# Performance work log

Measured on AMD Instinct MI355X. Metric: run time of the kernel, lower is better.

## Reference

```python
import jax, jax.numpy as jnp
import numpy as np

COST_KEYPOINT = 1.0
COST_GIOU = 1.0


def box_cxcyczwhd_to_xyzxyz(b):
    c, s = b[..., :3], b[..., 3:]
    return jnp.concatenate([c - 0.5 * s, c + 0.5 * s], axis=-1)


def generalized_3d_box_iou(b1, b2):
    # b1: [N,6], b2: [M,6], both xyzxyz. Returns [N,M] GIoU.
    vol1 = jnp.prod(b1[:, 3:] - b1[:, :3], axis=-1)
    vol2 = jnp.prod(b2[:, 3:] - b2[:, :3], axis=-1)
    lt = jnp.maximum(b1[:, None, :3], b2[None, :, :3])
    rb = jnp.minimum(b1[:, None, 3:], b2[None, :, 3:])
    inter = jnp.prod(jnp.maximum(rb - lt, 0.0), axis=-1)
    union = vol1[:, None] + vol2[None, :] - inter
    iou = inter / union
    elt = jnp.minimum(b1[:, None, :3], b2[None, :, :3])
    erb = jnp.maximum(b1[:, None, 3:], b2[None, :, 3:])
    evol = jnp.prod(jnp.maximum(erb - elt, 0.0), axis=-1)
    return iou - (evol - union) / evol


@jax.jit
def compute_cost(pred_keypoints, pred_boxes, tgt_boxes, tgt_keypoints):
    bs, Q = pred_keypoints.shape[:2]
    out_kp = pred_keypoints.reshape(bs * Q, -1)            # [bs*Q, K*3]
    out_boxes = pred_boxes.reshape(bs * Q, 6)
    tgt_b = tgt_boxes.reshape(-1, 6)                        # [T_total, 6]
    tgt_kp = tgt_keypoints.reshape(tgt_b.shape[0], -1)      # [T_total, K*3]
    xyz_min = box_cxcyczwhd_to_xyzxyz(tgt_b)[:, :3]
    K3 = tgt_kp.shape[-1]
    kp = tgt_kp.reshape(-1, K3 // 3, 3)
    # normalize keypoints relative to box min-corner and box size
    dist_kp = ((kp - xyz_min[:, None, :]) / tgt_b[:, None, 3:]).reshape(-1, K3)
    # L1 cdist: [bs*Q, T_total]
    cost_kp = jnp.sum(jnp.abs(out_kp[:, None, :] - dist_kp[None, :, :]), axis=-1)
    cost_giou = -generalized_3d_box_iou(
        box_cxcyczwhd_to_xyzxyz(out_boxes), box_cxcyczwhd_to_xyzxyz(tgt_b))
    C = COST_KEYPOINT * cost_kp + COST_GIOU * cost_giou
    return C.reshape(bs, Q, -1)


def _lap(cost):
    # Jonker-Volgenant shortest-augmenting-path LAP (scipy-style).
    # cost: [n, m] with n <= m. Returns (arange(n), col4row).
    cost = np.asarray(cost, dtype=np.float64)
    n, m = cost.shape
    u = np.zeros(n)
    v = np.zeros(m)
    col4row = np.full(n, -1, np.int64)
    row4col = np.full(m, -1, np.int64)
    for curRow in range(n):
        path = np.full(m, -1, np.int64)
        SR = np.zeros(n, bool)
        SC = np.zeros(m, bool)
        shortest = np.full(m, np.inf)
        minVal = 0.0
        i = curRow
        sink = -1
        while sink == -1:
            SR[i] = True
            idx = np.where(~SC)[0]
            r = minVal + cost[i, idx] - u[i] - v[idx]
            better = r < shortest[idx]
            shortest[idx[better]] = r[better]
            path[idx[better]] = i
            jloc = np.argmin(shortest[idx])
            j = idx[jloc]
            minVal = shortest[j]
            SC[j] = True
            if row4col[j] == -1:
                sink = j
            else:
                i = row4col[j]
        u[curRow] += minVal
        mask = SR.copy()
        mask[curRow] = False
        u[mask] += minVal - shortest[col4row[mask]]
        v[SC] -= minVal - shortest[SC]
        j = sink
        while True:
            i = path[j]
            row4col[j] = i
            col4row[i], j = j, col4row[i]
            if i == curRow:
                break
    return np.arange(n), col4row


def _linear_sum_assignment(cost):
    # cost: [Q, T] with Q >= T; mirrors scipy's transpose handling:
    # returns (row_ind sorted ascending, matching col_ind).
    rows, cols = _lap(cost.T)  # rows = arange(T) targets, cols = query ids
    order = np.argsort(cols)
    return cols[order], rows[order]


def setup_inputs() -> dict:
    key = jax.random.key(0)
    k1, k2, k3, k4, k5, k6 = jax.random.split(key, 6)
    BS, Q, T, K = 16, 300, 50, 17
    pred_keypoints = jax.random.normal(k1, (BS, Q, K * 3), dtype=jnp.float32)
    pred_boxes = jnp.concatenate([
        jax.random.uniform(k2, (BS, Q, 3), dtype=jnp.float32),
        jax.random.uniform(k3, (BS, Q, 3), dtype=jnp.float32) * 0.5 + 0.05,
    ], axis=-1)
    tgt_boxes = jnp.concatenate([
        jax.random.uniform(k4, (BS, T, 3), dtype=jnp.float32),
        jax.random.uniform(k5, (BS, T, 3), dtype=jnp.float32) * 0.5 + 0.05,
    ], axis=-1)
    tgt_keypoints = jax.random.uniform(k6, (BS, T, K * 3), dtype=jnp.float32)
    return {"pred_keypoints": pred_keypoints, "pred_boxes": pred_boxes,
            "tgt_boxes": tgt_boxes, "tgt_keypoints": tgt_keypoints}


def reference(pred_keypoints, pred_boxes, tgt_boxes, tgt_keypoints):
    C = compute_cost(pred_keypoints, pred_boxes, tgt_boxes, tgt_keypoints)
    Cn = np.asarray(C)
    bs, Q, _ = Cn.shape
    T = tgt_boxes.shape[1]
    # per-image block of the column-split cost matrix, as in torch C.split(sizes, -1)
    idx = []
    for b in range(bs):
        i, j = _linear_sum_assignment(Cn[b, :, b * T:(b + 1) * T])
        idx.append(np.stack([i, j]))
    indices = jnp.asarray(np.stack(idx), dtype=jnp.int32)  # [bs, 2, T]
    return C, indices
```

## Files before the change

kernel.cpp:

```cpp
#include <hip/hip_runtime.h>
#include <math.h>

#define BSZ 16
#define NQ 300
#define NT 50
#define K3 51
#define NPRED (BSZ*NQ)
#define NTGT  (BSZ*NT)
#define NC    (NPRED*NTGT)

template<int CTRL, int RMASK>
__device__ __forceinline__ double dpp_minstep_f64(double x) {
    long long bb = __double_as_longlong(x);
    int lo = (int)(bb & 0xFFFFFFFFll);
    int hi = (int)(bb >> 32);
    int mlo = __builtin_amdgcn_update_dpp(lo, lo, CTRL, RMASK, 0xF, false);
    int mhi = __builtin_amdgcn_update_dpp(hi, hi, CTRL, RMASK, 0xF, false);
    double other = __longlong_as_double(((long long)mhi << 32) | (long long)(unsigned)mlo);
    return fmin(x, other);
}
__device__ __forceinline__ double wave_min_f64(double x) {
    x = dpp_minstep_f64<0xB1, 0xF>(x);
    x = dpp_minstep_f64<0x4E, 0xF>(x);
    x = dpp_minstep_f64<0x141, 0xF>(x);
    x = dpp_minstep_f64<0x140, 0xF>(x);
    x = dpp_minstep_f64<0x142, 0xA>(x);
    x = dpp_minstep_f64<0x143, 0xC>(x);
    long long bb = __double_as_longlong(x);
    int lo = __builtin_amdgcn_readlane((int)(bb & 0xFFFFFFFFll), 63);
    int hi = __builtin_amdgcn_readlane((int)(bb >> 32), 63);
    return __longlong_as_double(((long long)hi << 32) | (long long)(unsigned)lo);
}
template<int CTRL, int RMASK>
__device__ __forceinline__ float dpp_minstep_f32(float x) {
    int m = __builtin_amdgcn_update_dpp(__float_as_int(x), __float_as_int(x), CTRL, RMASK, 0xF, false);
    return fminf(x, __int_as_float(m));
}
__device__ __forceinline__ float wave_min_f32(float x) {
    x = dpp_minstep_f32<0xB1, 0xF>(x);
    x = dpp_minstep_f32<0x4E, 0xF>(x);
    x = dpp_minstep_f32<0x141, 0xF>(x);
    x = dpp_minstep_f32<0x140, 0xF>(x);
    x = dpp_minstep_f32<0x142, 0xA>(x);
    x = dpp_minstep_f32<0x143, 0xC>(x);
    return __int_as_float(__builtin_amdgcn_readlane(__float_as_int(x), 63));
}
__device__ __forceinline__ double readlane_f64(double x, int lane) {
    long long bb = __double_as_longlong(x);
    int lo = __builtin_amdgcn_readlane((int)(bb & 0xFFFFFFFFll), lane);
    int hi = __builtin_amdgcn_readlane((int)(bb >> 32), lane);
    return __longlong_as_double(((long long)hi << 32) | (long long)(unsigned)lo);
}

__device__ __forceinline__ float giou_cost(
    float plt0, float plt1, float plt2, float prb0, float prb1, float prb2, float pvol,
    float tlt0, float tlt1, float tlt2, float trb0, float trb1, float trb2, float tvol)
{
    float inter = fmaxf(fminf(prb0,trb0) - fmaxf(plt0,tlt0), 0.f);
    inter *= fmaxf(fminf(prb1,trb1) - fmaxf(plt1,tlt1), 0.f);
    inter *= fmaxf(fminf(prb2,trb2) - fmaxf(plt2,tlt2), 0.f);
    float evol = fmaxf(fmaxf(prb0,trb0) - fminf(plt0,tlt0), 0.f);
    evol *= fmaxf(fmaxf(prb1,trb1) - fminf(plt1,tlt1), 0.f);
    evol *= fmaxf(fmaxf(prb2,trb2) - fminf(plt2,tlt2), 0.f);
    float uni = pvol + tvol - inter;
    return inter/uni - (evol - uni)/evol;
}

__global__ __launch_bounds__(1024) void cost_kernel(
    const float* __restrict__ pred_kp, const float* __restrict__ pred_boxes,
    const float* __restrict__ tgt_boxes, const float* __restrict__ tgt_kp,
    float* __restrict__ C, float* __restrict__ wsT)
{
    __shared__ __align__(16) float s_dk[80*56];
    __shared__ float s_tbox[80*12];
    __shared__ float s_pk[64*K3];

    const int cb = blockIdx.x;
    const int pb = cb % 75, tb = cb / 75;
    const int p0 = pb * 64, t0 = tb * 80;
    const int tid = threadIdx.x;

    if (tid < 80) {
        const float* tb6 = tgt_boxes + (size_t)(t0 + tid) * 6;
        float c0=tb6[0], c1=tb6[1], c2=tb6[2], s0=tb6[3], s1=tb6[4], s2=tb6[5];
        float l0=c0-0.5f*s0, l1=c1-0.5f*s1, l2=c2-0.5f*s2;
        float r0=c0+0.5f*s0, r1=c1+0.5f*s1, r2=c2+0.5f*s2;
        float* tw = s_tbox + tid*12;
        tw[0]=l0; tw[1]=l1; tw[2]=l2; tw[3]=r0; tw[4]=r1; tw[5]=r2;
        tw[6]=(r0-l0)*(r1-l1)*(r2-l2);
        tw[9]=s0; tw[10]=s1; tw[11]=s2;
    }
    __syncthreads();
    for (int e = tid; e < 80*K3; e += 1024) {
        int t = e / K3; int c = e - t*K3; int d = c % 3;
        float kp = tgt_kp[(size_t)t0*K3 + e];
        s_dk[t*56 + c] = (kp - s_tbox[t*12 + d]) / s_tbox[t*12 + 9 + d];
    }
    for (int e = tid; e < 64*K3; e += 1024)
        s_pk[e] = pred_kp[(size_t)p0*K3 + e];
    __syncthreads();

    const int pl = tid & 63, g = tid >> 6;
    float a[K3];
    #pragma unroll
    for (int c = 0; c < K3; ++c) a[c] = s_pk[pl*K3 + c];
    const int p = p0 + pl;
    const float* pb6 = pred_boxes + (size_t)p * 6;
    float pc0=pb6[0],pc1=pb6[1],pc2=pb6[2],ps0=pb6[3],ps1=pb6[4],ps2=pb6[5];
    float plt0=pc0-0.5f*ps0, plt1=pc1-0.5f*ps1, plt2=pc2-0.5f*ps2;
    float prb0=pc0+0.5f*ps0, prb1=pc1+0.5f*ps1, prb2=pc2+0.5f*ps2;
    float pvol=(prb0-plt0)*(prb1-plt1)*(prb2-plt2);
    const int bb2  = p / NQ;
    const int prel = p - bb2*NQ;

    #pragma unroll
    for (int k = 0; k < 5; ++k) {
        int tl = g*5 + k;
        const float* bbp = s_dk + tl*56;
        float sum = 0.f;
        #pragma unroll
        for (int c4 = 0; c4 < 12; ++c4) {
            float4 q = *(const float4*)(bbp + 4*c4);
            sum += fabsf(a[4*c4+0] - q.x);
            sum += fabsf(a[4*c4+1] - q.y);
            sum += fabsf(a[4*c4+2] - q.z);
            sum += fabsf(a[4*c4+3] - q.w);
        }
        sum += fabsf(a[48] - bbp[48]);
        sum += fabsf(a[49] - bbp[49]);
        sum += fabsf(a[50] - bbp[50]);
        const float* tw = s_tbox + tl*12;
        float g_ = giou_cost(plt0,plt1,plt2,prb0,prb1,prb2,pvol,
                             tw[0],tw[1],tw[2],tw[3],tw[4],tw[5],tw[6]);
        float val = sum - g_;
        C[(size_t)p*NTGT + (t0+tl)] = val;
        int trel = (t0+tl) - bb2*NT;
        if (trel >= 0 && trel < NT)
            wsT[bb2*(NT*NQ) + trel*NQ + prel] = val;
    }
}

__global__ __launch_bounds__(64) void lap_kernel(const float* __restrict__ wsT,
                                                 float* __restrict__ out_idx)
{
    const int b  = blockIdx.x;
    const int ln = threadIdx.x;
    const float* gt = wsT + b*(NT*NQ);

    float t0_[NT], t1_[NT], t2_[NT], t3_[NT], t4_[NT];
    const int q4 = (ln < 44) ? (ln + 256) : 0;
    #pragma unroll
    for (int r = 0; r < NT; ++r) {
        t0_[r] = gt[r*NQ + ln];
        t1_[r] = gt[r*NQ + ln + 64];
        t2_[r] = gt[r*NQ + ln + 128];
        t3_[r] = gt[r*NQ + ln + 192];
        t4_[r] = gt[r*NQ + q4];
    }

    const double DINF = __builtin_inf();
    double u = 0.0;
    int c4r = -1;
    double v[5], sh[5];
    int pth[5];
    #pragma unroll
    for (int s = 0; s < 5; ++s) v[s] = 0.0;

#define ROWC(I) case I: cfa[0]=t0_[I]; cfa[1]=t1_[I]; cfa[2]=t2_[I]; cfa[3]=t3_[I]; cfa[4]=t4_[I]; break;

    for (int curRow = 0; curRow < NT; ++curRow) {
        #pragma unroll
        for (int s = 0; s < 5; ++s) { sh[s] = DINF; pth[s] = -1; }
        int SCm = (ln < 44) ? 0 : 0x10;
        unsigned long long SRmask = 0ull;
        int i = curRow;
        double minVal = 0.0;
        int sink = -1;

        while (true) {
            SRmask |= (1ull << i);
            float cfa[5];
            switch (i) {
                ROWC(0)  ROWC(1)  ROWC(2)  ROWC(3)  ROWC(4)  ROWC(5)  ROWC(6)  ROWC(7)
                ROWC(8)  ROWC(9)  ROWC(10) ROWC(11) ROWC(12) ROWC(13) ROWC(14) ROWC(15)
                ROWC(16) ROWC(17) ROWC(18) ROWC(19) ROWC(20) ROWC(21) ROWC(22) ROWC(23)
                ROWC(24) ROWC(25) ROWC(26) ROWC(27) ROWC(28) ROWC(29) ROWC(30) ROWC(31)
                ROWC(32) ROWC(33) ROWC(34) ROWC(35) ROWC(36) ROWC(37) ROWC(38) ROWC(39)
                ROWC(40) ROWC(41) ROWC(42) ROWC(43) ROWC(44) ROWC(45) ROWC(46) ROWC(47)
                ROWC(48) ROWC(49)
                default: cfa[0]=cfa[1]=cfa[2]=cfa[3]=cfa[4]=0.f; break;
            }
            double u_i = readlane_f64(u, i);
            double lmin = DINF;
            #pragma unroll
            for (int s = 0; s < 5; ++s) {
                bool open = ((SCm >> s) & 1) == 0;
                double r = ((minVal + (double)cfa[s]) - u_i) - v[s];
                bool upd = open && (r < sh[s]);
                sh[s]  = upd ? r : sh[s];
                pth[s] = upd ? i : pth[s];
                lmin = fmin(lmin, open ? sh[s] : DINF);
            }
            float k32 = (float)lmin;
            float m32 = wave_min_f32(k32);
            unsigned long long candm = __ballot(k32 == m32);
            double m;
            if (__popcll(candm) == 1) {
                m = readlane_f64(lmin, (int)__builtin_ctzll(candm));
            } else {
                m = wave_min_f64(lmin);
            }
            minVal = m;
            unsigned long long b0 = __ballot((((SCm >> 0) & 1) == 0) && (sh[0] == m));
            unsigned long long b1 = __ballot((((SCm >> 1) & 1) == 0) && (sh[1] == m));
            unsigned long long b2 = __ballot((((SCm >> 2) & 1) == 0) && (sh[2] == m));
            unsigned long long b3 = __ballot((((SCm >> 3) & 1) == 0) && (sh[3] == m));
            unsigned long long b4 = __ballot((((SCm >> 4) & 1) == 0) && (sh[4] == m));
            int jstar;
            if      (b0) jstar =       __builtin_ctzll(b0);
            else if (b1) jstar =  64 + __builtin_ctzll(b1);
            else if (b2) jstar = 128 + __builtin_ctzll(b2);
            else if (b3) jstar = 192 + __builtin_ctzll(b3);
            else         jstar = 256 + __builtin_ctzll(b4);
            if (ln == (jstar & 63)) SCm |= 1 << (jstar >> 6);
            unsigned long long mm = __ballot((ln < NT) && (c4r == jstar));
            if (mm == 0ull) { sink = jstar; break; }
            i = __builtin_ctzll(mm);
        }

        int cg  = (c4r >= 0) ? c4r : 0;
        int gow = cg & 63, gsl = cg >> 6;
        double g0 = __shfl(sh[0], gow);
        double g1 = __shfl(sh[1], gow);
        double g2 = __shfl(sh[2], gow);
        double g3 = __shfl(sh[3], gow);
        double g4 = __shfl(sh[4], gow);
        double gg = g0;
        gg = (gsl == 1) ? g1 : gg;
        gg = (gsl == 2) ? g2 : gg;
        gg = (gsl == 3) ? g3 : gg;
        gg = (gsl == 4) ? g4 : gg;
        bool inSR = (ln < NT) && ((SRmask >> ln) & 1ull);
        double du = (ln == curRow) ? minVal : (minVal - gg);
        u = inSR ? (u + du) : u;
        #pragma unroll
        for (int s = 0; s < 5; ++s) {
            bool closed = ((SCm >> s) & 1) != 0;
            v[s] = closed ? (v[s] - (minVal - sh[s])) : v[s];
        }

        int j = sink;
        while (true) {
            int ow2 = j & 63, sl2 = j >> 6;
            int ps = pth[0];
            ps = (sl2==1) ? pth[1] : ps;
            ps = (sl2==2) ? pth[2] : ps;
            ps = (sl2==3) ? pth[3] : ps;
            ps = (sl2==4) ? pth[4] : ps;
            int ii = __builtin_amdgcn_readlane(ps, ow2);
            int jj = __builtin_amdgcn_readlane(c4r, ii);
            if (ln == ii) c4r = j;
            j = jj;
            if (ii == curRow) break;
        }
    }

    __shared__ int smem_i[NT];
    if (ln < NT) smem_i[ln] = c4r;
    __syncthreads();
    int myc = c4r;
    int rank = 0;
    for (int s2 = 0; s2 < NT; ++s2) rank += (smem_i[s2] < myc) ? 1 : 0;
    if (ln < NT) {
        out_idx[b*(2*NT) + rank]      = (float)myc;
        out_idx[b*(2*NT) + NT + rank] = (float)ln;
    }
}

extern "C" void kernel_launch(void* const* d_in, const int* in_sizes, int n_in,
                              void* d_out, int out_size, void* d_ws, size_t ws_size,
                              hipStream_t stream)
{
    const float* pred_kp    = (const float*)d_in[0];
    const float* pred_boxes = (const float*)d_in[1];
    const float* tgt_boxes  = (const float*)d_in[2];
    const float* tgt_kp     = (const float*)d_in[3];
    float* C   = (float*)d_out;
    float* idx = C + NC;
    float* wsT = (float*)d_ws;

    cost_kernel<<<750, 1024, 0, stream>>>(pred_kp, pred_boxes, tgt_boxes, tgt_kp, C, wsT);
    lap_kernel<<<BSZ, 64, 0, stream>>>(wsT, idx);
}
```

Baseline: 159.5 us.

## Stage cost tile in LDS for coalesced stores; drop transposed workspace copy

The cost kernel now writes its 64x80 output tile into padded shared memory and then stores it to C with coalesced row-contiguous writes, instead of each thread writing strided columns. The separate transposed per-batch workspace copy is removed, and the LAP kernel reads its diagonal block directly from C with strided loads. This cuts the extra scattered stores in the cost kernel, but it makes the LAP kernel's initial loads strided across rows of C (stride of 800 floats), which may be slower for that single-wave-per-batch kernel.

```diff
diff --git a/kernel.cpp b/kernel.cpp
--- a/kernel.cpp
+++ b/kernel.cpp
@@ -69,11 +69,12 @@
 __global__ __launch_bounds__(1024) void cost_kernel(
     const float* __restrict__ pred_kp, const float* __restrict__ pred_boxes,
     const float* __restrict__ tgt_boxes, const float* __restrict__ tgt_kp,
-    float* __restrict__ C, float* __restrict__ wsT)
+    float* __restrict__ C)
 {
     __shared__ __align__(16) float s_dk[80*56];
     __shared__ float s_tbox[80*12];
     __shared__ float s_pk[64*K3];
+    __shared__ float s_out[64*81];
 
     const int cb = blockIdx.x;
     const int pb = cb % 75, tb = cb / 75;
@@ -110,8 +111,6 @@
     float plt0=pc0-0.5f*ps0, plt1=pc1-0.5f*ps1, plt2=pc2-0.5f*ps2;
     float prb0=pc0+0.5f*ps0, prb1=pc1+0.5f*ps1, prb2=pc2+0.5f*ps2;
     float pvol=(prb0-plt0)*(prb1-plt1)*(prb2-plt2);
-    const int bb2  = p / NQ;
-    const int prel = p - bb2*NQ;
 
     #pragma unroll
     for (int k = 0; k < 5; ++k) {
@@ -132,30 +131,32 @@
         const float* tw = s_tbox + tl*12;
         float g_ = giou_cost(plt0,plt1,plt2,prb0,prb1,prb2,pvol,
                              tw[0],tw[1],tw[2],tw[3],tw[4],tw[5],tw[6]);
-        float val = sum - g_;
-        C[(size_t)p*NTGT + (t0+tl)] = val;
-        int trel = (t0+tl) - bb2*NT;
-        if (trel >= 0 && trel < NT)
-            wsT[bb2*(NT*NQ) + trel*NQ + prel] = val;
-    }
-}
-
-__global__ __launch_bounds__(64) void lap_kernel(const float* __restrict__ wsT,
-                                                 float* __restrict__ out_idx)
+        s_out[pl*81 + tl] = sum - g_;
+    }
+    __syncthreads();
+
+    for (int e = tid; e < 64*80; e += 1024) {
+        int pp = e / 80, t = e - pp*80;
+        C[(size_t)(p0+pp)*NTGT + (t0+t)] = s_out[pp*81 + t];
+    }
+}
+
+__global__ __launch_bounds__(64, 1) void lap_kernel(const float* __restrict__ C,
+                                                    float* __restrict__ out_idx)
 {
     const int b  = blockIdx.x;
     const int ln = threadIdx.x;
-    const float* gt = wsT + b*(NT*NQ);
+    const float* gC = C + (size_t)(b*NQ)*NTGT + b*NT;
 
     float t0_[NT], t1_[NT], t2_[NT], t3_[NT], t4_[NT];
-    const int q4 = (ln < 44) ? (ln + 256) : 0;
+    const int j4 = (ln < 44) ? (ln + 256) : 0;
     #pragma unroll
     for (int r = 0; r < NT; ++r) {
-        t0_[r] = gt[r*NQ + ln];
-        t1_[r] = gt[r*NQ + ln + 64];
-        t2_[r] = gt[r*NQ + ln + 128];
-        t3_[r] = gt[r*NQ + ln + 192];
-        t4_[r] = gt[r*NQ + q4];
+        t0_[r] = gC[(size_t)(ln      )*NTGT + r];
+        t1_[r] = gC[(size_t)(ln +  64)*NTGT + r];
+        t2_[r] = gC[(size_t)(ln + 128)*NTGT + r];
+        t3_[r] = gC[(size_t)(ln + 192)*NTGT + r];
+        t4_[r] = gC[(size_t)(j4      )*NTGT + r];
     }
 
     const double DINF = __builtin_inf();
@@ -287,8 +288,7 @@
     const float* tgt_kp     = (const float*)d_in[3];
     float* C   = (float*)d_out;
     float* idx = C + NC;
-    float* wsT = (float*)d_ws;
-
-    cost_kernel<<<750, 1024, 0, stream>>>(pred_kp, pred_boxes, tgt_boxes, tgt_kp, C, wsT);
-    lap_kernel<<<BSZ, 64, 0, stream>>>(wsT, idx);
-}
+
+    cost_kernel<<<750, 1024, 0, stream>>>(pred_kp, pred_boxes, tgt_boxes, tgt_kp, C);
+    lap_kernel<<<BSZ, 64, 0, stream>>>(C, idx);
+}
```

Result: slower. 167.5 us (+5.0%).
